# Kernel tuning notes

Hardware: AMD Instinct MI355X
Metric: run time of the kernel (lower is better)

Reference implementation:

```python
import jax, jax.numpy as jnp
import numpy as np

B, S, HID = 2, 2048, 3584
H, KV, D = 16, 8, 256
RQ, RK, RV = 6, 2, 2
GRP = H // KV
EPS = 1e-6
SOFTCAP = 50.0
SCALE = 256.0 ** -0.5  # query_pre_attn_scalar ** -0.5
NEG = -2.3819763e38


def _rmsnorm(x, w):
    # Gemma RMSNorm: fp32 normalize, scale by (1 + weight)
    xf = x.astype(jnp.float32)
    n = xf * jax.lax.rsqrt(jnp.mean(xf * xf, axis=-1, keepdims=True) + EPS)
    return (n * (1.0 + w)).astype(x.dtype)


def _rope_factor(x, freqs_cis):
    # x: [B,S,R,D]; freqs_cis: [S, D/2, 2] = (cos, sin)
    h = D // 2
    cos = freqs_cis[None, :, None, :, 0]  # [1,S,1,D/2]
    sin = freqs_cis[None, :, None, :, 1]
    x1, x2 = x[..., :h], x[..., h:]
    return jnp.concatenate([x1 * cos - x2 * sin, x2 * cos + x1 * sin], axis=-1)


def setup_inputs() -> dict:
    key = jax.random.key(0)
    ks = jax.random.split(key, 10)
    hidden_states = jax.random.normal(ks[0], (B, S, HID), dtype=jnp.float32)
    # rotary tables
    pos = jnp.arange(S, dtype=jnp.float32)
    inv = 1.0 / (10000.0 ** (jnp.arange(0, D, 2, dtype=jnp.float32) / D))
    ang = pos[:, None] * inv[None, :]                     # [S, D/2]
    freqs_cis = jnp.stack([jnp.cos(ang), jnp.sin(ang)], axis=-1)  # [S,D/2,2]
    kv_write_indices = jnp.arange(S, dtype=jnp.int32)
    k_cache_A = jnp.zeros((B, S, KV, RK), jnp.float32)
    k_cache_B = jnp.zeros((B, S, RK, D), jnp.float32)
    v_cache_A = jnp.zeros((B, S, KV, RV), jnp.float32)
    v_cache_B = jnp.zeros((B, S, RV, D), jnp.float32)
    causal = jnp.tril(jnp.ones((S, S), bool))
    mask = jnp.where(causal, 0.0, NEG)[None, None].astype(jnp.float32)
    sd = 1.0 / np.sqrt(HID)
    W_A_q = jax.random.normal(ks[1], (HID, H * RQ), jnp.float32) * sd
    W_A_k = jax.random.normal(ks[2], (HID, KV * RK), jnp.float32) * sd
    W_A_v = jax.random.normal(ks[3], (HID, KV * RV), jnp.float32) * sd
    W_B_q = jax.random.normal(ks[4], (HID, RQ * D), jnp.float32) * sd
    W_B_k = jax.random.normal(ks[5], (HID, RK * D), jnp.float32) * sd
    W_B_v = jax.random.normal(ks[6], (HID, RV * D), jnp.float32) * sd
    o_proj_w = jax.random.normal(ks[7], (H * D, HID), jnp.float32) * (1.0 / np.sqrt(H * D))
    q_norm_w = jnp.zeros((D,), jnp.float32)
    k_norm_w = jnp.zeros((D,), jnp.float32)
    return dict(hidden_states=hidden_states, freqs_cis=freqs_cis,
                kv_write_indices=kv_write_indices,
                k_cache_A=k_cache_A, k_cache_B=k_cache_B,
                v_cache_A=v_cache_A, v_cache_B=v_cache_B, mask=mask,
                W_A_q=W_A_q, W_A_k=W_A_k, W_A_v=W_A_v,
                W_B_q=W_B_q, W_B_k=W_B_k, W_B_v=W_B_v,
                o_proj_w=o_proj_w, q_norm_w=q_norm_w, k_norm_w=k_norm_w)


def reference(hidden_states, freqs_cis, kv_write_indices,
              k_cache_A, k_cache_B, v_cache_A, v_cache_B, mask,
              W_A_q, W_A_k, W_A_v, W_B_q, W_B_k, W_B_v,
              o_proj_w, q_norm_w, k_norm_w):
    hs = hidden_states
    # rank-factor projections (many small GEMMs)
    A_q = (hs @ W_A_q).reshape(B, S, H, RQ)
    A_k = (hs @ W_A_k).reshape(B, S, KV, RK)
    A_v = (hs @ W_A_v).reshape(B, S, KV, RV)
    B_q = (hs @ W_B_q).reshape(B, S, RQ, D)
    B_k = (hs @ W_B_k).reshape(B, S, RK, D)
    B_v = (hs @ W_B_v).reshape(B, S, RV, D)
    # qk-norm on low-rank B factors
    B_q = _rmsnorm(B_q, q_norm_w)
    B_k = _rmsnorm(B_k, k_norm_w)
    # RoPE on factors
    B_q = _rope_factor(B_q, freqs_cis)
    B_k = _rope_factor(B_k, freqs_cis)
    # factored KV cache write (prefill: indices = arange(S))
    kA = k_cache_A.at[:, kv_write_indices].set(A_k)
    kB = k_cache_B.at[:, kv_write_indices].set(B_k)
    vA = v_cache_A.at[:, kv_write_indices].set(A_v)
    vB = v_cache_B.at[:, kv_write_indices].set(B_v)
    # reconstruct Q/K/V from rank-R tensor products, divided by rank
    Q = jnp.einsum('bshr,bsrd->bshd', A_q.astype(jnp.float32),
                   B_q.astype(jnp.float32)) / RQ          # [B,S,H,D]
    K = jnp.einsum('bskr,bsrd->bskd', kA, kB) / RK        # [B,S,KV,D]
    V = jnp.einsum('bskr,bsrd->bskd', vA, vB) / RV
    Q = Q.astype(hs.dtype)
    # GQA expand
    K = jnp.repeat(K, GRP, axis=2)
    V = jnp.repeat(V, GRP, axis=2)
    q = jnp.transpose(Q, (0, 2, 1, 3)) * SCALE            # [B,H,S,D]
    k = jnp.transpose(K, (0, 2, 1, 3))
    v = jnp.transpose(V, (0, 2, 1, 3))
    scores = jnp.einsum('bhqd,bhkd->bhqk', q, k).astype(jnp.float32)
    scores = SOFTCAP * jnp.tanh(scores / SOFTCAP)
    scores = scores + mask
    probs = jax.nn.softmax(scores, axis=-1).astype(q.dtype)
    out = jnp.einsum('bhqk,bhkd->bhqd', probs, v)         # [B,H,S,D]
    out = jnp.transpose(out, (0, 2, 1, 3)).reshape(B, S, H * D)
    return out @ o_proj_w
```

## Files before the change

### kernel.cpp

```cpp
#include <hip/hip_runtime.h>

#define B_    2
#define S_    2048
#define HID_  3584
#define H_    16
#define KV_   8
#define D_    256
#define RQ_   6
#define NPROJ 2688
#define HD_   4096
#define MTOK  4096
#define EPS_  1e-6f
#define NEG_  -2.3819763e38f
#define SCALE_ 0.0625f

typedef unsigned short u16;
typedef __attribute__((ext_vector_type(8))) short short8;
typedef __attribute__((ext_vector_type(4))) float f32x4;

__device__ __forceinline__ u16 f2bf(float f) {
  unsigned u = __float_as_uint(f);
  u += 0x7fffu + ((u >> 16) & 1u);
  return (u16)(u >> 16);
}

__device__ __forceinline__ void gl_lds16(const void* g, void* l) {
  __builtin_amdgcn_global_load_lds((__attribute__((address_space(1))) void*)g,
                                   (__attribute__((address_space(3))) void*)l, 16, 0, 0);
}

__global__ __launch_bounds__(256) void cvt_f32_bf16(const float* __restrict__ src,
                                                    u16* __restrict__ dst, int n) {
  int i = blockIdx.x * 256 + threadIdx.x;
  const int stride = gridDim.x * 256;
  const int n4 = n >> 2;
  for (; i < n4; i += stride) {
    float4 v = ((const float4*)src)[i];
    ushort4 o;
    o.x = f2bf(v.x); o.y = f2bf(v.y); o.z = f2bf(v.z); o.w = f2bf(v.w);
    ((ushort4*)dst)[i] = o;
  }
}

__global__ __launch_bounds__(256) void transpose_f32_bf16(const float* __restrict__ src,
                                                          u16* __restrict__ dst, int R, int C) {
  __shared__ float tile[32][33];
  const int tx = threadIdx.x & 31, ty = threadIdx.x >> 5;
  const int r0 = blockIdx.x << 5, c0 = blockIdx.y << 5;
#pragma unroll
  for (int j = 0; j < 4; ++j) {
    int r = r0 + ty + j * 8, c = c0 + tx;
    tile[ty + j * 8][tx] = (r < R && c < C) ? src[(size_t)r * C + c] : 0.f;
  }
  __syncthreads();
#pragma unroll
  for (int j = 0; j < 4; ++j) {
    int cc = c0 + ty + j * 8, rr = r0 + tx;
    if (cc < C && rr < R) dst[(size_t)cc * R + rr] = f2bf(tile[tx][ty + j * 8]);
  }
}

__global__ __launch_bounds__(256) void transpose_bf16_b(const u16* __restrict__ src,
                                                        u16* __restrict__ dst, int R, int C) {
  __shared__ u16 tile[32][34];
  const size_t plane = (size_t)R * C;
  const u16* s = src + (size_t)blockIdx.z * plane;
  u16* d = dst + (size_t)blockIdx.z * plane;
  const int tx = threadIdx.x & 31, ty = threadIdx.x >> 5;
  const int r0 = blockIdx.x << 5, c0 = blockIdx.y << 5;
#pragma unroll
  for (int j = 0; j < 4; ++j) {
    int r = r0 + ty + j * 8, c = c0 + tx;
    tile[ty + j * 8][tx] = (r < R && c < C) ? s[(size_t)r * C + c] : (u16)0;
  }
  __syncthreads();
#pragma unroll
  for (int j = 0; j < 4; ++j) {
    int cc = c0 + ty + j * 8, rr = r0 + tx;
    if (cc < C && rr < R) d[(size_t)cc * R + rr] = tile[tx][ty + j * 8];
  }
}

__global__ __launch_bounds__(256, 2)
void gemm_bt(const u16* __restrict__ A, const u16* __restrict__ Bm, float* __restrict__ C,
             int M, int N, int K, int lda, int ldb, int ldc) {
  __shared__ __align__(16) u16 As[2][4096];
  __shared__ __align__(16) u16 Bs[2][4096];
  const int t = threadIdx.x;
  const int lane = t & 63;
  const int lq = lane & 15, lg = lane >> 4;
  const int wid = t >> 6;
  const int wr = wid >> 1, wc = wid & 1;
  const int m0 = blockIdx.x * 128, n0 = blockIdx.y * 128;

  const int row0 = t >> 2;
  const int row1 = 64 + row0;
  const int sl = t & 3;
  const char* ga0 = (const char*)(A + (size_t)(m0 + row0) * lda) + ((sl ^ ((row0 >> 1) & 3)) << 4);
  const char* ga1 = (const char*)(A + (size_t)(m0 + row1) * lda) + ((sl ^ ((row1 >> 1) & 3)) << 4);
  const char* gb0 = (const char*)(Bm + (size_t)(n0 + row0) * ldb) + ((sl ^ ((row0 >> 1) & 3)) << 4);
  const char* gb1 = (const char*)(Bm + (size_t)(n0 + row1) * ldb) + ((sl ^ ((row1 >> 1) & 3)) << 4);
  u16* Abase = &As[0][0];
  u16* Bbase = &Bs[0][0];
  const int ldst0 = t * 8, ldst1 = 2048 + t * 8;

  int aoff[4], boff[4];
#pragma unroll
  for (int i = 0; i < 4; ++i) {
    int ra = wr * 64 + i * 16 + lq;
    aoff[i] = ra * 32 + ((lg ^ ((ra >> 1) & 3)) << 3);
    int rb = wc * 64 + i * 16 + lq;
    boff[i] = rb * 32 + ((lg ^ ((rb >> 1) & 3)) << 3);
  }

  f32x4 zero = {0.f, 0.f, 0.f, 0.f};
  f32x4 acc[4][4];
#pragma unroll
  for (int i = 0; i < 4; ++i)
#pragma unroll
    for (int j = 0; j < 4; ++j) acc[i][j] = zero;

  const int nk = K >> 5;
  gl_lds16(ga0, Abase + ldst0);
  gl_lds16(ga1, Abase + ldst1);
  gl_lds16(gb0, Bbase + ldst0);
  gl_lds16(gb1, Bbase + ldst1);
  __syncthreads();
  int cur = 0;
  for (int kt = 0; kt < nk; ++kt) {
    if (kt + 1 < nk) {
      const size_t ko = (size_t)(kt + 1) * 64;
      const int nb = (cur ^ 1) * 4096;
      gl_lds16(ga0 + ko, Abase + nb + ldst0);
      gl_lds16(ga1 + ko, Abase + nb + ldst1);
      gl_lds16(gb0 + ko, Bbase + nb + ldst0);
      gl_lds16(gb1 + ko, Bbase + nb + ldst1);
    }
    const int cb = cur * 4096;
    short8 af[4], bfr[4];
#pragma unroll
    for (int i = 0; i < 4; ++i) {
      af[i] = *(const short8*)(Abase + cb + aoff[i]);
      bfr[i] = *(const short8*)(Bbase + cb + boff[i]);
    }
#pragma unroll
    for (int i = 0; i < 4; ++i)
#pragma unroll
      for (int j = 0; j < 4; ++j)
        acc[i][j] = __builtin_amdgcn_mfma_f32_16x16x32_bf16(af[i], bfr[j], acc[i][j], 0, 0, 0);
    __syncthreads();
    cur ^= 1;
  }
#pragma unroll
  for (int i = 0; i < 4; ++i)
#pragma unroll
    for (int j = 0; j < 4; ++j) {
      const int row = m0 + wr * 64 + i * 16 + lg * 4;
      const int col = n0 + wc * 64 + j * 16 + lq;
      float* cp = C + (size_t)row * ldc + col;
#pragma unroll
      for (int r = 0; r < 4; ++r) cp[(size_t)r * ldc] = acc[i][j][r];
    }
}

__global__ __launch_bounds__(256)
void build_qkv(const float* __restrict__ P, const float* __restrict__ freqs,
               const float* __restrict__ qw, const float* __restrict__ kw,
               u16* __restrict__ Qg, u16* __restrict__ Kg, u16* __restrict__ Vg) {
  const int token = blockIdx.x;
  const int b = token >> 11, s = token & 2047;
  const int d = threadIdx.x;
  const float* row = P + (size_t)token * NPROJ;
  __shared__ float aL[128];
  __shared__ float rQ[6][256];
  __shared__ float rK[2][256];
  __shared__ float red[4][8];

  if (d < 128) aL[d] = row[d];
  float bq[6], bk[2], bv[2];
#pragma unroll
  for (int r = 0; r < 6; ++r) bq[r] = row[128 + r * 256 + d];
#pragma unroll
  for (int r = 0; r < 2; ++r) bk[r] = row[1664 + r * 256 + d];
#pragma unroll
  for (int r = 0; r < 2; ++r) bv[r] = row[2176 + r * 256 + d];

  float sq[8];
#pragma unroll
  for (int r = 0; r < 6; ++r) sq[r] = bq[r] * bq[r];
  sq[6] = bk[0] * bk[0];
  sq[7] = bk[1] * bk[1];
#pragma unroll
  for (int j = 0; j < 8; ++j) {
    sq[j] += __shfl_xor(sq[j], 32, 64);
    sq[j] += __shfl_xor(sq[j], 16, 64);
    sq[j] += __shfl_xor(sq[j], 8, 64);
    sq[j] += __shfl_xor(sq[j], 4, 64);
    sq[j] += __shfl_xor(sq[j], 2, 64);
    sq[j] += __shfl_xor(sq[j], 1, 64);
  }
  const int lane = d & 63, wv = d >> 6;
  if (lane == 0) {
#pragma unroll
    for (int j = 0; j < 8; ++j) red[wv][j] = sq[j];
  }
  __syncthreads();
  float inv[8];
#pragma unroll
  for (int j = 0; j < 8; ++j) {
    float ss = red[0][j] + red[1][j] + red[2][j] + red[3][j];
    inv[j] = rsqrtf(ss * (1.0f / 256.0f) + EPS_);
  }
  const float gq = 1.f + qw[d], gk = 1.f + kw[d];
#pragma unroll
  for (int r = 0; r < 6; ++r) rQ[r][d] = bq[r] * inv[r] * gq;
#pragma unroll
  for (int r = 0; r < 2; ++r) rK[r][d] = bk[r] * inv[6 + r] * gk;
  __syncthreads();

  const int dh = d & 127;
  const float co = freqs[(s * 128 + dh) * 2 + 0];
  const float sn = freqs[(s * 128 + dh) * 2 + 1];
  float q_ro[6], k_ro[2];
  if (d < 128) {
#pragma unroll
    for (int r = 0; r < 6; ++r) q_ro[r] = rQ[r][d] * co - rQ[r][d + 128] * sn;
#pragma unroll
    for (int r = 0; r < 2; ++r) k_ro[r] = rK[r][d] * co - rK[r][d + 128] * sn;
  } else {
#pragma unroll
    for (int r = 0; r < 6; ++r) q_ro[r] = rQ[r][d] * co + rQ[r][d - 128] * sn;
#pragma unroll
    for (int r = 0; r < 2; ++r) k_ro[r] = rK[r][d] * co + rK[r][d - 128] * sn;
  }
  const float qs = SCALE_ * (1.0f / 6.0f);
#pragma unroll
  for (int h = 0; h < 16; ++h) {
    float a = 0.f;
#pragma unroll
    for (int r = 0; r < 6; ++r) a += aL[h * 6 + r] * q_ro[r];
    Qg[((size_t)(b * H_ + h) * S_ + s) * D_ + d] = f2bf(a * qs);
  }
#pragma unroll
  for (int kv = 0; kv < 8; ++kv) {
    float ak = aL[96 + kv * 2] * k_ro[0] + aL[96 + kv * 2 + 1] * k_ro[1];
    Kg[((size_t)(b * KV_ + kv) * S_ + s) * D_ + d] = f2bf(ak * 0.5f);
    float av = aL[112 + kv * 2] * bv[0] + aL[112 + kv * 2 + 1] * bv[1];
    Vg[((size_t)(b * KV_ + kv) * S_ + s) * D_ + d] = f2bf(av * 0.5f);
  }
}

__global__ __launch_bounds__(256, 2)
void attn_kernel(const u16* __restrict__ Qg, const u16* __restrict__ Kg,
                 const u16* __restrict__ VTg, u16* __restrict__ Og) {
  __shared__ __align__(16) u16 Kbuf[2][8192];
  __shared__ __align__(16) u16 Vbuf[2][8192];
  __shared__ __align__(16) u16 Pbuf[4][512];

  const int t = threadIdx.x;
  const int lane = t & 63;
  const int lq = lane & 15, lg = lane >> 4;
  const int qw = t >> 6;
  const int h = blockIdx.x, b = blockIdx.y;
  const int qt = 31 - blockIdx.z;
  const int q0 = qt * 64;
  const int kvh = h >> 1;

  const u16* Kplane = Kg + (size_t)(b * KV_ + kvh) * S_ * D_;
  const u16* VTplane = VTg + (size_t)(b * KV_ + kvh) * D_ * S_;

  const int qg = q0 + qw * 16 + lq;
  const u16* Qrow = Qg + ((size_t)(b * H_ + h) * S_ + qg) * D_;
  short8 qf[8];
#pragma unroll
  for (int ks = 0; ks < 8; ++ks) qf[ks] = *(const short8*)(Qrow + ks * 32 + lg * 8);

  int ksrc[4], vsrc[4];
#pragma unroll
  for (int i = 0; i < 4; ++i) {
    const int kr = i * 8 + (t >> 5);
    ksrc[i] = kr * D_ + (((t & 31) ^ (kr & 7)) << 3);
    const int vr = i * 64 + (t >> 2);
    vsrc[i] = vr * S_ + (((t & 3) ^ ((vr >> 1) & 3)) << 3);
  }

  f32x4 zero = {0.f, 0.f, 0.f, 0.f};
  f32x4 oacc[16];
#pragma unroll
  for (int db = 0; db < 16; ++db) oacc[db] = zero;
  float m_s = NEG_, l_s = 0.f;

  const int qro = q0 + qw * 16 + lg * 4;
  const int nt = 2 * (qt + 1);

#pragma unroll
  for (int i = 0; i < 4; ++i) {
    gl_lds16(Kplane + ksrc[i], &Kbuf[0][0] + (i * 256 + t) * 8);
    gl_lds16(VTplane + vsrc[i], &Vbuf[0][0] + (i * 256 + t) * 8);
  }
  __syncthreads();
  int cur = 0;
  for (int it = 0; it < nt; ++it) {
    const int kv0 = it * 32;
    if (it + 1 < nt) {
      const u16* kp = Kplane + (size_t)(it + 1) * 32 * D_;
      const u16* vp = VTplane + (it + 1) * 32;
      u16* kd = &Kbuf[cur ^ 1][0];
      u16* vd = &Vbuf[cur ^ 1][0];
#pragma unroll
      for (int i = 0; i < 4; ++i) {
        gl_lds16(kp + ksrc[i], kd + (i * 256 + t) * 8);
        gl_lds16(vp + vsrc[i], vd + (i * 256 + t) * 8);
      }
    }
    const u16* Kb = &Kbuf[cur][0];
    f32x4 sacc[2];
    sacc[0] = zero; sacc[1] = zero;
    __builtin_amdgcn_s_setprio(1);
#pragma unroll
    for (int kb = 0; kb < 2; ++kb) {
      const int rbase = (kb * 16 + lq) * 256;
      const int sw = lq & 7;
#pragma unroll
      for (int ks = 0; ks < 8; ++ks) {
        short8 kf = *(const short8*)(Kb + rbase + (((ks * 4 + lg) ^ sw) << 3));
        sacc[kb] = __builtin_amdgcn_mfma_f32_16x16x32_bf16(kf, qf[ks], sacc[kb], 0, 0, 0);
      }
    }
    __builtin_amdgcn_s_setprio(0);
    const bool tail = (it >= 2 * qt);
#pragma unroll
    for (int kb = 0; kb < 2; ++kb)
#pragma unroll
      for (int r = 0; r < 4; ++r) {
        float x = sacc[kb][r];
        const float e = __expf(-fabsf(x) * 0.04f);
        const float th = (1.f - e) * __builtin_amdgcn_rcpf(1.f + e);
        x = copysignf(50.0f * th, x);
        if (tail && (kv0 + kb * 16 + lg * 4 + r > qg)) x = NEG_;
        sacc[kb][r] = x;
      }
    float vmax = fmaxf(fmaxf(fmaxf(sacc[0][0], sacc[0][1]), fmaxf(sacc[0][2], sacc[0][3])),
                       fmaxf(fmaxf(sacc[1][0], sacc[1][1]), fmaxf(sacc[1][2], sacc[1][3])));
    vmax = fmaxf(vmax, __shfl_xor(vmax, 16, 64));
    vmax = fmaxf(vmax, __shfl_xor(vmax, 32, 64));
    if (__any(vmax > m_s + 8.f)) {
      const float mn = fmaxf(m_s, vmax);
      const float c = __expf(m_s - mn);
      m_s = mn;
      l_s *= c;
      float c4[4];
#pragma unroll
      for (int r = 0; r < 4; ++r) c4[r] = __shfl(c, lg * 4 + r, 16);
#pragma unroll
      for (int db = 0; db < 16; ++db) {
        oacc[db][0] *= c4[0]; oacc[db][1] *= c4[1];
        oacc[db][2] *= c4[2]; oacc[db][3] *= c4[3];
      }
    }
    float ps = 0.f;
#pragma unroll
    for (int kb = 0; kb < 2; ++kb)
#pragma unroll
      for (int r = 0; r < 4; ++r) {
        const float p = __expf(sacc[kb][r] - m_s);
        sacc[kb][r] = p;
        ps += p;
      }
    ps += __shfl_xor(ps, 16, 64);
    ps += __shfl_xor(ps, 32, 64);
    l_s += ps;
    u16* Pw = &Pbuf[qw][0];
#pragma unroll
    for (int kb = 0; kb < 2; ++kb) {
      ushort4 pk;
      pk.x = f2bf(sacc[kb][0]); pk.y = f2bf(sacc[kb][1]);
      pk.z = f2bf(sacc[kb][2]); pk.w = f2bf(sacc[kb][3]);
      *(ushort4*)(Pw + 8 * lq + 128 * (2 * kb + (lg >> 1)) + 4 * (lg & 1)) = pk;
    }
    short8 pf = *(const short8*)(Pw + lane * 8);
    const u16* Vb = &Vbuf[cur][0];
    __builtin_amdgcn_s_setprio(1);
#pragma unroll
    for (int db = 0; db < 16; ++db) {
      const int d = db * 16 + lq;
      short8 vf = *(const short8*)(Vb + d * 32 + ((lg ^ ((lq >> 1) & 3)) << 3));
      oacc[db] = __builtin_amdgcn_mfma_f32_16x16x32_bf16(pf, vf, oacc[db], 0, 0, 0);
    }
    __builtin_amdgcn_s_setprio(0);
    __syncthreads();
    cur ^= 1;
  }
  const float invl = __builtin_amdgcn_rcpf(l_s);
  float inv4[4];
#pragma unroll
  for (int r = 0; r < 4; ++r) inv4[r] = __shfl(invl, lg * 4 + r, 16);
#pragma unroll
  for (int r = 0; r < 4; ++r) {
    u16* orow = Og + (size_t)(b * S_ + qro + r) * HD_ + h * D_;
#pragma unroll
    for (int db = 0; db < 16; ++db) orow[db * 16 + lq] = f2bf(oacc[db][r] * inv4[r]);
  }
}

extern "C" void kernel_launch(void* const* d_in, const int* in_sizes, int n_in,
                              void* d_out, int out_size, void* d_ws, size_t ws_size,
                              hipStream_t stream) {
  const float* hs    = (const float*)d_in[0];
  const float* freqs = (const float*)d_in[1];
  const float* W_A_q = (const float*)d_in[8];
  const float* W_A_k = (const float*)d_in[9];
  const float* W_A_v = (const float*)d_in[10];
  const float* W_B_q = (const float*)d_in[11];
  const float* W_B_k = (const float*)d_in[12];
  const float* W_B_v = (const float*)d_in[13];
  const float* Wo    = (const float*)d_in[14];
  const float* qw    = (const float*)d_in[15];
  const float* kw    = (const float*)d_in[16];
  float* out = (float*)d_out;

  char* ws = (char*)d_ws;
  u16* hsb = (u16*)(ws);
  u16* WT  = (u16*)(ws + 29360128);
  u16* WoT = (u16*)(ws + 48627712);
  u16* Qg  = (u16*)(ws + 77987840);
  u16* Kg  = (u16*)(ws + 111542272);
  u16* Vg  = (u16*)(ws + 128319488);
  u16* VTg = (u16*)(ws + 145096704);
  u16* AOg = (u16*)(ws + 161873920);
  float* Pout = (float*)d_out;

  cvt_f32_bf16<<<1024, 256, 0, stream>>>(hs, hsb, MTOK * HID_);
  transpose_f32_bf16<<<dim3(112, 3),   256, 0, stream>>>(W_A_q, WT + (size_t)0 * HID_,    HID_, 96);
  transpose_f32_bf16<<<dim3(112, 1),   256, 0, stream>>>(W_A_k, WT + (size_t)96 * HID_,   HID_, 16);
  transpose_f32_bf16<<<dim3(112, 1),   256, 0, stream>>>(W_A_v, WT + (size_t)112 * HID_,  HID_, 16);
  transpose_f32_bf16<<<dim3(112, 48),  256, 0, stream>>>(W_B_q, WT + (size_t)128 * HID_,  HID_, 1536);
  transpose_f32_bf16<<<dim3(112, 16),  256, 0, stream>>>(W_B_k, WT + (size_t)1664 * HID_, HID_, 512);
  transpose_f32_bf16<<<dim3(112, 16),  256, 0, stream>>>(W_B_v, WT + (size_t)2176 * HID_, HID_, 512);
  transpose_f32_bf16<<<dim3(128, 112), 256, 0, stream>>>(Wo, WoT, HD_, HID_);

  gemm_bt<<<dim3(32, 21), 256, 0, stream>>>(hsb, WT, Pout, MTOK, NPROJ, HID_, HID_, HID_, NPROJ);
  build_qkv<<<4096, 256, 0, stream>>>(Pout, freqs, qw, kw, Qg, Kg, Vg);
  transpose_bf16_b<<<dim3(64, 8, 16), 256, 0, stream>>>(Vg, VTg, S_, D_);
  attn_kernel<<<dim3(16, 2, 32), 256, 0, stream>>>(Qg, Kg, VTg, AOg);
  gemm_bt<<<dim3(32, 28), 256, 0, stream>>>(AOg, WoT, out, MTOK, HID_, HD_, HD_, HD_, HID_);
}
```

Baseline: 470.0 us.

## Replace 128x128 GEMM with 256x256-tile, 512-thread pipelined MFMA GEMM

Replaces both projection GEMMs with a kernel that computes 256x256 output tiles using 8 waves, each owning a 128x64 sub-tile. Global-to-LDS loads are split into k-halves and interleaved with MFMA groups, using explicit vmcnt waits, raw barriers and s_setprio. The goal is more operand reuse per LDS byte and better overlap of memory traffic with matrix math. In exchange the kernel holds more accumulator registers, and the N=2688 GEMM needs column bounds checks plus a padded final tile that fetches rows past the end of WT.

```diff
diff --git a/kernel.cpp b/kernel.cpp
--- a/kernel.cpp
+++ b/kernel.cpp
@@ -81,86 +81,140 @@
   }
 }
 
-__global__ __launch_bounds__(256, 2)
-void gemm_bt(const u16* __restrict__ A, const u16* __restrict__ Bm, float* __restrict__ C,
-             int M, int N, int K, int lda, int ldb, int ldc) {
-  __shared__ __align__(16) u16 As[2][4096];
-  __shared__ __align__(16) u16 Bs[2][4096];
+__global__ __launch_bounds__(512, 2)
+void gemm256(const u16* __restrict__ A, const u16* __restrict__ Bm, float* __restrict__ C,
+             int N, int lda, int ldb, int ldc, int NT) {
+  __shared__ __align__(16) u16 lds[2][2][2][8192];
   const int t = threadIdx.x;
   const int lane = t & 63;
   const int lq = lane & 15, lg = lane >> 4;
-  const int wid = t >> 6;
-  const int wr = wid >> 1, wc = wid & 1;
-  const int m0 = blockIdx.x * 128, n0 = blockIdx.y * 128;
-
-  const int row0 = t >> 2;
-  const int row1 = 64 + row0;
-  const int sl = t & 3;
-  const char* ga0 = (const char*)(A + (size_t)(m0 + row0) * lda) + ((sl ^ ((row0 >> 1) & 3)) << 4);
-  const char* ga1 = (const char*)(A + (size_t)(m0 + row1) * lda) + ((sl ^ ((row1 >> 1) & 3)) << 4);
-  const char* gb0 = (const char*)(Bm + (size_t)(n0 + row0) * ldb) + ((sl ^ ((row0 >> 1) & 3)) << 4);
-  const char* gb1 = (const char*)(Bm + (size_t)(n0 + row1) * ldb) + ((sl ^ ((row1 >> 1) & 3)) << 4);
-  u16* Abase = &As[0][0];
-  u16* Bbase = &Bs[0][0];
-  const int ldst0 = t * 8, ldst1 = 2048 + t * 8;
-
-  int aoff[4], boff[4];
-#pragma unroll
-  for (int i = 0; i < 4; ++i) {
-    int ra = wr * 64 + i * 16 + lq;
-    aoff[i] = ra * 32 + ((lg ^ ((ra >> 1) & 3)) << 3);
-    int rb = wc * 64 + i * 16 + lq;
-    boff[i] = rb * 32 + ((lg ^ ((rb >> 1) & 3)) << 3);
-  }
+  const int w = t >> 6;
+  const int wm = w >> 2, wn = w & 3;
+  const int bm0 = blockIdx.x * 256, bn0 = blockIdx.y * 256;
+
+  const int rsub = lane >> 2;
+  const int ksub = ((lane & 3) << 3) ^ ((lane >> 5) << 4);
+  const u16* pa0 = A + (size_t)(bm0 + w * 16 + rsub) * lda + ksub;
+  const u16* pa1 = pa0 + (size_t)128 * lda;
+  const u16* pb0 = Bm + (size_t)(bn0 + w * 16 + rsub) * ldb + ksub;
+  const u16* pb1 = pb0 + (size_t)128 * ldb;
+
+  const int rdo = lq * 32 + ((lg << 3) ^ (((lq >> 3) & 1) << 4));
+  const int bsub = (wn & 1) << 3;
 
   f32x4 zero = {0.f, 0.f, 0.f, 0.f};
-  f32x4 acc[4][4];
-#pragma unroll
-  for (int i = 0; i < 4; ++i)
-#pragma unroll
-    for (int j = 0; j < 4; ++j) acc[i][j] = zero;
-
-  const int nk = K >> 5;
-  gl_lds16(ga0, Abase + ldst0);
-  gl_lds16(ga1, Abase + ldst1);
-  gl_lds16(gb0, Bbase + ldst0);
-  gl_lds16(gb1, Bbase + ldst1);
-  __syncthreads();
+  f32x4 acc[8][4];
+#pragma unroll
+  for (int m = 0; m < 8; ++m)
+#pragma unroll
+    for (int n = 0; n < 4; ++n) acc[m][n] = zero;
+
+  gl_lds16(pa0,      &lds[0][0][0][(w * 2 + 0) * 512]);
+  gl_lds16(pa1,      &lds[0][0][1][(w * 2 + 0) * 512]);
+  gl_lds16(pb0,      &lds[0][1][0][(w * 2 + 0) * 512]);
+  gl_lds16(pb1,      &lds[0][1][1][(w * 2 + 0) * 512]);
+  gl_lds16(pa0 + 32, &lds[0][0][0][(w * 2 + 1) * 512]);
+  gl_lds16(pa1 + 32, &lds[0][0][1][(w * 2 + 1) * 512]);
+  gl_lds16(pb0 + 32, &lds[0][1][0][(w * 2 + 1) * 512]);
+  gl_lds16(pb1 + 32, &lds[0][1][1][(w * 2 + 1) * 512]);
+
   int cur = 0;
-  for (int kt = 0; kt < nk; ++kt) {
-    if (kt + 1 < nk) {
-      const size_t ko = (size_t)(kt + 1) * 64;
-      const int nb = (cur ^ 1) * 4096;
-      gl_lds16(ga0 + ko, Abase + nb + ldst0);
-      gl_lds16(ga1 + ko, Abase + nb + ldst1);
-      gl_lds16(gb0 + ko, Bbase + nb + ldst0);
-      gl_lds16(gb1 + ko, Bbase + nb + ldst1);
-    }
-    const int cb = cur * 4096;
-    short8 af[4], bfr[4];
-#pragma unroll
-    for (int i = 0; i < 4; ++i) {
-      af[i] = *(const short8*)(Abase + cb + aoff[i]);
-      bfr[i] = *(const short8*)(Bbase + cb + boff[i]);
-    }
-#pragma unroll
-    for (int i = 0; i < 4; ++i)
-#pragma unroll
-      for (int j = 0; j < 4; ++j)
-        acc[i][j] = __builtin_amdgcn_mfma_f32_16x16x32_bf16(af[i], bfr[j], acc[i][j], 0, 0, 0);
-    __syncthreads();
+  for (int T = 0; T < NT; ++T) {
+    const bool pre = (T + 1) < NT;
+    const size_t ko = (size_t)(T + 1) * 64;
+    const u16* ab = &lds[cur][0][wm][0];
+    const u16* bb = &lds[cur][1][wn >> 1][0];
+    const int nb = cur ^ 1;
+
+    asm volatile("s_waitcnt vmcnt(4)" ::: "memory");
+    __builtin_amdgcn_s_barrier();
+    __builtin_amdgcn_sched_barrier(0);
+    short8 af[4], bf[4];
+#pragma unroll
+    for (int m = 0; m < 4; ++m) af[m] = *(const short8*)(ab + (m * 2 + 0) * 512 + rdo);
+#pragma unroll
+    for (int n = 0; n < 4; ++n) bf[n] = *(const short8*)(bb + (bsub + n * 2 + 0) * 512 + rdo);
+    if (pre) {
+      gl_lds16(pa0 + ko, &lds[nb][0][0][(w * 2 + 0) * 512]);
+      gl_lds16(pa1 + ko, &lds[nb][0][1][(w * 2 + 0) * 512]);
+    }
+    __builtin_amdgcn_s_setprio(1);
+#pragma unroll
+    for (int m = 0; m < 4; ++m)
+#pragma unroll
+      for (int n = 0; n < 4; ++n)
+        acc[m][n] = __builtin_amdgcn_mfma_f32_16x16x32_bf16(af[m], bf[n], acc[m][n], 0, 0, 0);
+    __builtin_amdgcn_s_setprio(0);
+
+    short8 ag[4];
+#pragma unroll
+    for (int m = 0; m < 4; ++m) ag[m] = *(const short8*)(ab + ((m + 4) * 2 + 0) * 512 + rdo);
+    if (pre) {
+      gl_lds16(pb0 + ko, &lds[nb][1][0][(w * 2 + 0) * 512]);
+      gl_lds16(pb1 + ko, &lds[nb][1][1][(w * 2 + 0) * 512]);
+    }
+    __builtin_amdgcn_s_setprio(1);
+#pragma unroll
+    for (int m = 0; m < 4; ++m)
+#pragma unroll
+      for (int n = 0; n < 4; ++n)
+        acc[m + 4][n] = __builtin_amdgcn_mfma_f32_16x16x32_bf16(ag[m], bf[n], acc[m + 4][n], 0, 0, 0);
+    __builtin_amdgcn_s_setprio(0);
+
+    if (pre) { asm volatile("s_waitcnt vmcnt(4)" ::: "memory"); }
+    else     { asm volatile("s_waitcnt vmcnt(0)" ::: "memory"); }
+    __builtin_amdgcn_s_barrier();
+    __builtin_amdgcn_sched_barrier(0);
+    short8 af2[4], bf2[4];
+#pragma unroll
+    for (int m = 0; m < 4; ++m) af2[m] = *(const short8*)(ab + (m * 2 + 1) * 512 + rdo);
+#pragma unroll
+    for (int n = 0; n < 4; ++n) bf2[n] = *(const short8*)(bb + (bsub + n * 2 + 1) * 512 + rdo);
+    if (pre) {
+      gl_lds16(pa0 + ko + 32, &lds[nb][0][0][(w * 2 + 1) * 512]);
+      gl_lds16(pa1 + ko + 32, &lds[nb][0][1][(w * 2 + 1) * 512]);
+    }
+    __builtin_amdgcn_s_setprio(1);
+#pragma unroll
+    for (int m = 0; m < 4; ++m)
+#pragma unroll
+      for (int n = 0; n < 4; ++n)
+        acc[m][n] = __builtin_amdgcn_mfma_f32_16x16x32_bf16(af2[m], bf2[n], acc[m][n], 0, 0, 0);
+    __builtin_amdgcn_s_setprio(0);
+
+    short8 ag2[4];
+#pragma unroll
+    for (int m = 0; m < 4; ++m) ag2[m] = *(const short8*)(ab + ((m + 4) * 2 + 1) * 512 + rdo);
+    if (pre) {
+      gl_lds16(pb0 + ko + 32, &lds[nb][1][0][(w * 2 + 1) * 512]);
+      gl_lds16(pb1 + ko + 32, &lds[nb][1][1][(w * 2 + 1) * 512]);
+    }
+    __builtin_amdgcn_s_setprio(1);
+#pragma unroll
+    for (int m = 0; m < 4; ++m)
+#pragma unroll
+      for (int n = 0; n < 4; ++n)
+        acc[m + 4][n] = __builtin_amdgcn_mfma_f32_16x16x32_bf16(ag2[m], bf2[n], acc[m + 4][n], 0, 0, 0);
+    __builtin_amdgcn_s_setprio(0);
+
     cur ^= 1;
   }
-#pragma unroll
-  for (int i = 0; i < 4; ++i)
-#pragma unroll
-    for (int j = 0; j < 4; ++j) {
-      const int row = m0 + wr * 64 + i * 16 + lg * 4;
-      const int col = n0 + wc * 64 + j * 16 + lq;
-      float* cp = C + (size_t)row * ldc + col;
-#pragma unroll
-      for (int r = 0; r < 4; ++r) cp[(size_t)r * ldc] = acc[i][j][r];
-    }
+
+#pragma unroll
+  for (int m = 0; m < 8; ++m) {
+    const int row = bm0 + wm * 128 + m * 16 + lg * 4;
+#pragma unroll
+    for (int n = 0; n < 4; ++n) {
+      const int col = bn0 + wn * 64 + n * 16 + lq;
+      if (col < N) {
+        float* cp = C + (size_t)row * ldc + col;
+        cp[0] = acc[m][n][0];
+        cp[(size_t)ldc] = acc[m][n][1];
+        cp[(size_t)2 * ldc] = acc[m][n][2];
+        cp[(size_t)3 * ldc] = acc[m][n][3];
+      }
+    }
+  }
 }
 
 __global__ __launch_bounds__(256)
@@ -439,9 +493,9 @@
   transpose_f32_bf16<<<dim3(112, 16),  256, 0, stream>>>(W_B_v, WT + (size_t)2176 * HID_, HID_, 512);
   transpose_f32_bf16<<<dim3(128, 112), 256, 0, stream>>>(Wo, WoT, HD_, HID_);
 
-  gemm_bt<<<dim3(32, 21), 256, 0, stream>>>(hsb, WT, Pout, MTOK, NPROJ, HID_, HID_, HID_, NPROJ);
+  gemm256<<<dim3(16, 11), 512, 0, stream>>>(hsb, WT, Pout, NPROJ, HID_, HID_, NPROJ, 56);
   build_qkv<<<4096, 256, 0, stream>>>(Pout, freqs, qw, kw, Qg, Kg, Vg);
   transpose_bf16_b<<<dim3(64, 8, 16), 256, 0, stream>>>(Vg, VTg, S_, D_);
   attn_kernel<<<dim3(16, 2, 32), 256, 0, stream>>>(Qg, Kg, VTg, AOg);
-  gemm_bt<<<dim3(32, 28), 256, 0, stream>>>(AOg, WoT, out, MTOK, HID_, HD_, HD_, HD_, HID_);
-}
+  gemm256<<<dim3(16, 14), 512, 0, stream>>>(AOg, WoT, out, HID_, HD_, HD_, HID_, 64);
+}
```

After: 431.4 us. -8.2%, faster.
